# Optimization experiments

Measured on AMD Instinct MI355X. Metric: run time of the kernel, lower is better.

## Reference

```python
import jax, jax.numpy as jnp
import numpy as np
from jax import lax

KS = 2          # kernel_size (even, so padding=ks/2 makes unfold/fold L match)
PAD = 1         # padding = ks//2
STRIDE = 1      # unfold stride
C_IN = 64
PATCH = KS * KS * C_IN  # 256


def unfold(x, ks, stride, pad):
    # torch.nn.functional.unfold ordering: channel-major, then kernel row, kernel col;
    # L axis is row-major over output positions. Output [B, C*ks*ks, L].
    xp = jnp.pad(x, ((0, 0), (0, 0), (pad, pad), (pad, pad)))
    B, C, H, W = xp.shape
    oh = (H - ks) // stride + 1
    ow = (W - ks) // stride + 1
    pats = jnp.stack(
        [xp[:, :, i:i + stride * oh:stride, j:j + stride * ow:stride]
         for i in range(ks) for j in range(ks)], axis=2)  # [B, C, ks*ks, oh, ow]
    return pats.reshape(B, C * ks * ks, oh * ow)


def fold(cols, Ho, Wo, ks, stride, pad):
    # inverse of unfold: scatter-add patch columns back onto an image.
    B, P, L = cols.shape
    C = P // (ks * ks)
    nb = (Ho + 2 * pad - ks) // stride + 1  # blocks per spatial dim
    cols = cols.reshape(B, C, ks, ks, nb, nb)
    out = jnp.zeros((B, C, Ho + 2 * pad, Wo + 2 * pad), dtype=cols.dtype)
    for ki in range(ks):
        for kj in range(ks):
            out = out.at[:, :, ki:ki + stride * nb:stride,
                         kj:kj + stride * nb:stride].add(cols[:, :, ki, kj])
    return out[:, :, pad:pad + Ho, pad:pad + Wo]


def setup_inputs() -> dict:
    key = jax.random.key(0)
    k1, k2, k3, k4 = jax.random.split(key, 4)
    x = jax.random.normal(k1, (32, C_IN, 56, 56), dtype=jnp.float32)
    weight = jax.random.normal(k2, (128, C_IN, KS, KS), dtype=jnp.float32) * 0.06
    bias = jax.random.normal(k3, (128,), dtype=jnp.float32) * 0.06
    cluster_centers = jax.random.uniform(k4, (512, PATCH), dtype=jnp.float32)
    temp = jnp.float32(1.0)
    return {"x": x, "weight": weight, "bias": bias,
            "cluster_centers": cluster_centers, "temp": temp}


def reference(x, weight, bias, cluster_centers, temp):
    B = x.shape[0]
    cols = unfold(x, KS, STRIDE, PAD)                  # [B, 256, L]
    Bc, P, L = cols.shape
    # faithful to torch: this_patch.view(-1, patch_size) on [B, P, L] (row-major)
    flat = cols.reshape(-1, PATCH)                      # [B*L, 256]
    # Euclidean cdist via gram trick
    x2 = jnp.sum(flat * flat, axis=-1, keepdims=True)   # [N,1]
    c2 = jnp.sum(cluster_centers * cluster_centers, axis=-1)  # [K]
    d = jnp.sqrt(jnp.maximum(x2 + c2 - 2.0 * (flat @ cluster_centers.T), 0.0))
    soft = jax.nn.softmax(-d * temp, axis=1)             # [N, K]
    transformed = soft @ cluster_centers                 # [N, 256]
    final = (temp * transformed + flat) / (temp + 1.0)
    final = final.reshape(Bc, P, L)
    new_size = x.shape[3] * KS                           # 112
    x_refold = fold(final, new_size, new_size, KS, KS, PAD)
    # F.conv2d(x_refold, weight, bias, stride=ks, padding=pad, dilation=groups=1)
    out = lax.conv_general_dilated(
        x_refold, weight, window_strides=(KS, KS),
        padding=[(PAD, PAD), (PAD, PAD)],
        dimension_numbers=("NCHW", "OIHW", "NCHW"))
    return out + bias[None, :, None, None]
```

## Files before the change

kernel.cpp:

```cpp
#include <hip/hip_runtime.h>
#include <stdint.h>

#define NB    32
#define CIN   64
#define HW    56
#define OHW   57
#define LL    3249
#define PATCH 256
#define NCENT 512
#define OC    128
#define NROWS (NB*LL)
#define NROWS_PAD 104064
#define PL    (PATCH*LL)

typedef __attribute__((ext_vector_type(8))) short short8;
typedef __attribute__((ext_vector_type(4))) float f32x4;
typedef __attribute__((ext_vector_type(4))) int   int4v;
typedef int int4u __attribute__((ext_vector_type(4), aligned(4)));
typedef __attribute__((ext_vector_type(4))) unsigned short ushort4v;
typedef __attribute__((ext_vector_type(8))) unsigned short ushort8;

constexpr size_t OFF_C2   = 0;
constexpr size_t OFF_X2   = 4096;
constexpr size_t OFF_DENP = OFF_X2 + (size_t)NROWS_PAD*4;
constexpr size_t OFF_DEN  = OFF_DENP + (size_t)8*NROWS_PAD*4;
constexpr size_t OFF_CBF  = OFF_DEN + (size_t)NROWS_PAD*4;
constexpr size_t OFF_CTBF = OFF_CBF + (size_t)NCENT*PATCH*2;
constexpr size_t OFF_WBF  = OFF_CTBF + (size_t)PATCH*NCENT*2;
constexpr size_t OFF_FLAT = OFF_WBF + (size_t)OC*PATCH*2;
constexpr size_t OFF_P    = OFF_FLAT + (size_t)NROWS_PAD*PATCH*2;
constexpr size_t OFF_FBM  = OFF_P + (size_t)NROWS_PAD*NCENT*2;

__device__ __forceinline__ short f2bf(float f) {
    union { float f; uint32_t u; } v; v.f = f;
    uint32_t r = (v.u + 0x7FFFu + ((v.u >> 16) & 1u)) >> 16;
    return (short)r;
}
__device__ __forceinline__ float bf2f(uint16_t h) {
    union { uint32_t u; float f; } v; v.u = ((uint32_t)h) << 16;
    return v.f;
}
__device__ __forceinline__ void gload16(const void* g, void* l) {
    __builtin_amdgcn_global_load_lds(
        (const __attribute__((address_space(1))) unsigned int*)g,
        (__attribute__((address_space(3))) unsigned int*)l, 16, 0, 0);
}

__global__ __launch_bounds__(256)
void k0a_centers(const float* __restrict__ centers, uint16_t* __restrict__ cbf,
                 uint16_t* __restrict__ ctbf, float* __restrict__ c2) {
    __shared__ float red[4];
    int c = blockIdx.x;
    int k = threadIdx.x;
    float v = centers[c*PATCH + k];
    cbf[c*PATCH + (k ^ ((c & 3) << 3))] = (uint16_t)f2bf(v);
    ctbf[k*NCENT + (c ^ ((k & 3) << 3))] = (uint16_t)f2bf(v);
    float s = v*v;
    s += __shfl_xor(s, 1);  s += __shfl_xor(s, 2);  s += __shfl_xor(s, 4);
    s += __shfl_xor(s, 8);  s += __shfl_xor(s, 16); s += __shfl_xor(s, 32);
    int w = threadIdx.x >> 6;
    if ((threadIdx.x & 63) == 0) red[w] = s;
    __syncthreads();
    if (threadIdx.x == 0) c2[c] = red[0] + red[1] + red[2] + red[3];
}

__global__ __launch_bounds__(256)
void k0w_weight(const float* __restrict__ weight, uint16_t* __restrict__ wbf) {
    int o = blockIdx.x, p = threadIdx.x;
    wbf[o*PATCH + (p ^ ((o & 7) << 3))] = (uint16_t)f2bf(weight[o*PATCH + p]);
}

__global__ __launch_bounds__(256)
void k0b_flat(const float* __restrict__ x, uint16_t* __restrict__ flat,
              float* __restrict__ x2) {
    int tid = threadIdx.x;
    int w = tid >> 6, lane = tid & 63;
    for (int pp = 0; pp < 8; ++pp) {
        int n = blockIdx.x*32 + pp*4 + w;
        int b = n / LL;
        int rr = n - b*LL;
        int k0 = lane*4;
        float s = 0.f;
        ushort4v pk;
#pragma unroll
        for (int e = 0; e < 4; ++e) {
            int k = k0 + e;
            float val = 0.f;
            if (n < NROWS) {
                int o = rr*PATCH + k;
                int p = o / LL; int l = o - p*LL;
                int cc = p >> 2, ki = (p >> 1) & 1, kj = p & 1;
                int i = l / OHW; int j = l - i*OHW;
                int y = i + ki - 1, xx = j + kj - 1;
                if ((unsigned)y < HW && (unsigned)xx < HW)
                    val = x[((b*CIN + cc)*HW + y)*HW + xx];
            }
            pk[e] = (unsigned short)f2bf(val);
            s += val*val;
        }
        *(ushort4v*)(flat + (size_t)n*PATCH + (k0 ^ ((n & 3) << 3))) = pk;
        s += __shfl_xor(s, 1);  s += __shfl_xor(s, 2);  s += __shfl_xor(s, 4);
        s += __shfl_xor(s, 8);  s += __shfl_xor(s, 16); s += __shfl_xor(s, 32);
        if (lane == 0) x2[n] = s;
    }
}

__global__ __launch_bounds__(256, 4)
void k1_scores(const uint16_t* __restrict__ flat, const uint16_t* __restrict__ cbf,
               const float* __restrict__ x2g, const float* __restrict__ c2g,
               const float* __restrict__ temp_p,
               uint16_t* __restrict__ P, float* __restrict__ denp) {
    __shared__ __align__(16) char lds[32768];
    const int tid = threadIdx.x;
    const int mt = blockIdx.x, nt = blockIdx.y;
    const int w = tid >> 6, lane = tid & 63;
    const int wr = w >> 1, wc = w & 1;
    const int l15 = lane & 15, l4 = lane >> 4;

    auto stage = [&](int buf, int kt) {
        const char* srcA = (const char*)flat + (size_t)(mt*128)*512 + kt*64;
        const char* srcB = (const char*)cbf + (size_t)(nt*128)*512 + kt*64;
        char* dA = lds + buf*16384;
        char* dB = dA + 8192;
#pragma unroll
        for (int i = 0; i < 2; ++i) {
            int u = (w*2 + i)*64 + lane;
            int row = u >> 2, sub = u & 3;
            gload16(srcA + (size_t)row*512 + sub*16, dA + u*16);
            gload16(srcB + (size_t)row*512 + sub*16, dB + u*16);
        }
    };

    f32x4 acc[4][4];
#pragma unroll
    for (int i = 0; i < 4; ++i)
#pragma unroll
        for (int j = 0; j < 4; ++j) acc[i][j] = (f32x4)0.f;

    stage(0, 0);
    for (int kt = 0; kt < 8; ++kt) {
        __syncthreads();
        if (kt < 7) stage((kt + 1) & 1, kt + 1);
        const char* A = lds + (kt & 1)*16384;
        const char* B = A + 8192;
        short8 af[4], bfm[4];
#pragma unroll
        for (int rf = 0; rf < 4; ++rf) {
            int row = wr*64 + rf*16 + l15;
            int byte = row*64 + ((l4*16) ^ ((row & 3) << 4));
            af[rf] = *(const short8*)(A + byte);
        }
#pragma unroll
        for (int cf = 0; cf < 4; ++cf) {
            int row = wc*64 + cf*16 + l15;
            int byte = row*64 + ((l4*16) ^ ((row & 3) << 4));
            bfm[cf] = *(const short8*)(B + byte);
        }
#pragma unroll
        for (int rf = 0; rf < 4; ++rf)
#pragma unroll
            for (int cf = 0; cf < 4; ++cf)
                acc[rf][cf] = __builtin_amdgcn_mfma_f32_16x16x32_bf16(
                    af[rf], bfm[cf], acc[rf][cf], 0, 0, 0);
    }

    const float temp = temp_p[0];
    float c2v[4];
#pragma unroll
    for (int cf = 0; cf < 4; ++cf)
        c2v[cf] = c2g[nt*128 + wc*64 + cf*16 + l15];

    float denacc[4][4];
#pragma unroll
    for (int rf = 0; rf < 4; ++rf) {
#pragma unroll
        for (int rr = 0; rr < 4; ++rr) {
            int n = mt*128 + wr*64 + rf*16 + l4*4 + rr;
            float x2v = x2g[n];
            float d = 0.f;
#pragma unroll
            for (int cf = 0; cf < 4; ++cf) {
                float s = x2v + c2v[cf] - 2.f*acc[rf][cf][rr];
                float pv = __expf(-temp * sqrtf(fmaxf(s, 0.f)));
                acc[rf][cf][rr] = pv;
                d += pv;
            }
            denacc[rf][rr] = d;
        }
    }
#pragma unroll
    for (int rf = 0; rf < 4; ++rf)
#pragma unroll
        for (int rr = 0; rr < 4; ++rr) {
            float v = denacc[rf][rr];
            v += __shfl_xor(v, 1); v += __shfl_xor(v, 2);
            v += __shfl_xor(v, 4); v += __shfl_xor(v, 8);
            if (l15 == 0) {
                int n = mt*128 + wr*64 + rf*16 + l4*4 + rr;
                denp[(size_t)(nt*2 + wc)*NROWS_PAD + n] = v;
            }
        }

    __syncthreads();
    uint16_t* Pl = (uint16_t*)lds;
#pragma unroll
    for (int rf = 0; rf < 4; ++rf)
#pragma unroll
        for (int cf = 0; cf < 4; ++cf)
#pragma unroll
            for (int rr = 0; rr < 4; ++rr) {
                int row = wr*64 + rf*16 + l4*4 + rr;
                int cl  = wc*64 + cf*16 + l15;
                Pl[row*128 + (cl ^ ((row & 3) << 3))] = (uint16_t)f2bf(acc[rf][cf][rr]);
            }
    __syncthreads();
#pragma unroll
    for (int i = 0; i < 8; ++i) {
        int c = i*256 + tid;
        int row = c >> 4, sub = c & 15;
        int4v v = *(const int4v*)((const char*)lds + c*16);
        *(int4v*)((char*)P + (size_t)(mt*128 + row)*1024 + nt*256 + sub*16) = v;
    }
}

__global__ __launch_bounds__(128)
void kden(const float* __restrict__ denp, float* __restrict__ den) {
    int n = blockIdx.x*128 + threadIdx.x;
    float s = 0.f;
#pragma unroll
    for (int p = 0; p < 8; ++p) s += denp[(size_t)p*NROWS_PAD + n];
    den[n] = s;
}

__global__ __launch_bounds__(256, 4)
void k2_pv(const uint16_t* __restrict__ P, const uint16_t* __restrict__ ctbf,
           const uint16_t* __restrict__ flat, const float* __restrict__ den,
           const float* __restrict__ temp_p, uint16_t* __restrict__ fbm) {
    __shared__ __align__(16) char lds[32768];
    const int tid = threadIdx.x;
    const int mt = blockIdx.x, nt = blockIdx.y;
    const int w = tid >> 6, lane = tid & 63;
    const int wr = w >> 1, wc = w & 1;
    const int l15 = lane & 15, l4 = lane >> 4;

    auto stage = [&](int buf, int kt) {
        const char* srcA = (const char*)P + (size_t)(mt*128)*1024 + kt*64;
        const char* srcB = (const char*)ctbf + (size_t)(nt*128)*1024 + kt*64;
        char* dA = lds + buf*16384;
        char* dB = dA + 8192;
#pragma unroll
        for (int i = 0; i < 2; ++i) {
            int u = (w*2 + i)*64 + lane;
            int row = u >> 2, sub = u & 3;
            gload16(srcA + (size_t)row*1024 + sub*16, dA + u*16);
            gload16(srcB + (size_t)row*1024 + sub*16, dB + u*16);
        }
    };

    f32x4 acc[4][4];
#pragma unroll
    for (int i = 0; i < 4; ++i)
#pragma unroll
        for (int j = 0; j < 4; ++j) acc[i][j] = (f32x4)0.f;

    stage(0, 0);
    for (int kt = 0; kt < 16; ++kt) {
        __syncthreads();
        if (kt < 15) stage((kt + 1) & 1, kt + 1);
        const char* A = lds + (kt & 1)*16384;
        const char* B = A + 8192;
        short8 af[4], bfm[4];
#pragma unroll
        for (int rf = 0; rf < 4; ++rf) {
            int row = wr*64 + rf*16 + l15;
            int byte = row*64 + ((l4*16) ^ ((row & 3) << 4));
            af[rf] = *(const short8*)(A + byte);
        }
#pragma unroll
        for (int cf = 0; cf < 4; ++cf) {
            int row = wc*64 + cf*16 + l15;
            int byte = row*64 + ((l4*16) ^ ((row & 3) << 4));
            bfm[cf] = *(const short8*)(B + byte);
        }
#pragma unroll
        for (int rf = 0; rf < 4; ++rf)
#pragma unroll
            for (int cf = 0; cf < 4; ++cf)
                acc[rf][cf] = __builtin_amdgcn_mfma_f32_16x16x32_bf16(
                    af[rf], bfm[cf], acc[rf][cf], 0, 0, 0);
    }

    __syncthreads();
    uint16_t* Tl = (uint16_t*)lds;
#pragma unroll
    for (int rf = 0; rf < 4; ++rf)
#pragma unroll
        for (int cf = 0; cf < 4; ++cf)
#pragma unroll
            for (int rr = 0; rr < 4; ++rr) {
                int row = wr*64 + rf*16 + l4*4 + rr;
                int col = wc*64 + cf*16 + l15;
                Tl[row*128 + (col ^ ((row & 7) << 3))] = (uint16_t)f2bf(acc[rf][cf][rr]);
            }
    __syncthreads();

    const float temp = temp_p[0];
    const float inv = 1.f / (temp + 1.f);
#pragma unroll
    for (int i = 0; i < 8; ++i) {
        int ch = i*256 + tid;
        int row = ch >> 4, m0 = (ch & 15)*8;
        int n = mt*128 + row;
        if (n >= NROWS) continue;
        int m = nt*128 + m0;
        float dv = den[n];
        float a1 = temp * inv / dv;
        ushort8 tvv = *(const ushort8*)(Tl + row*128 + (m0 ^ ((row & 7) << 3)));
        ushort8 fl = *(const ushort8*)(flat + (size_t)n*PATCH + (m ^ ((row & 3) << 3)));
        int b = n / LL;
        int rrow = n - b*LL;
        int o = rrow*PATCH + m;
        int p = o / LL; int l = o - p*LL;
        int ii = l / OHW; int jj = l - ii*OHW;
        ushort8 outv;
#pragma unroll
        for (int e = 0; e < 8; ++e) {
            int ki = (p >> 1) & 1, kj = p & 1;
            bool bad = (ii == 0 && ki == 0) || (ii == 56 && ki == 1) ||
                       (jj == 0 && kj == 0) || (jj == 56 && kj == 1);
            float fin = a1*bf2f(tvv[e]) + bf2f(fl[e])*inv;
            outv[e] = bad ? (unsigned short)0 : (unsigned short)f2bf(fin);
            if (++jj == OHW) { jj = 0; if (++ii == OHW) { ii = 0; ++p; } }
        }
        *(ushort8*)(fbm + (size_t)n*PATCH + m) = outv;
    }
}

__global__ __launch_bounds__(256, 2)
void k4_conv(const uint16_t* __restrict__ wbf, const uint16_t* __restrict__ fbm,
             const float* __restrict__ bias, float* __restrict__ out) {
    __shared__ __align__(16) char lds[2][32768];
    const int tid = threadIdx.x;
    const int lt = blockIdx.x;
    const int bb = blockIdx.y;
    const int w = tid >> 6, lane = tid & 63;
    const int wr = w >> 1, wc = w & 1;
    const int l15 = lane & 15, l4 = lane >> 4;

    auto stageA = [&](int buf, int kt) {
        const char* srcA = (const char*)wbf + kt*128;
        char* dA = lds[buf];
#pragma unroll
        for (int i = 0; i < 4; ++i) {
            int c = (w*4 + i)*64 + lane;
            gload16(srcA + (size_t)(c >> 3)*512 + (c & 7)*16, dA + (w*4 + i)*1024);
        }
    };
    auto stageB = [&](int buf, int kt) {
        uint16_t* sB = (uint16_t*)(lds[buf] + 16384);
#pragma unroll
        for (int i = 0; i < 4; ++i) {
            int pl = lane;
            int l8 = i*4 + w;
            const uint16_t* g = fbm + (size_t)bb*PL + (size_t)(kt*64 + pl)*LL + lt*128 + l8*8;
#pragma unroll
            for (int e = 0; e < 8; ++e) {
                uint16_t val = g[e];
                int llocal = l8*8 + e;
                sB[llocal*64 + (pl ^ (e << 3))] = val;
            }
        }
    };

    f32x4 acc[4][4];
#pragma unroll
    for (int i = 0; i < 4; ++i)
#pragma unroll
        for (int j = 0; j < 4; ++j) acc[i][j] = (f32x4)0.f;

    stageA(0, 0); stageB(0, 0);
    for (int kt = 0; kt < 4; ++kt) {
        __syncthreads();
        if (kt < 3) { stageA((kt + 1) & 1, kt + 1); stageB((kt + 1) & 1, kt + 1); }
        const char* A = lds[kt & 1];
        const char* B = lds[kt & 1] + 16384;
#pragma unroll
        for (int ks = 0; ks < 2; ++ks) {
            short8 af[4], bfm[4];
#pragma unroll
            for (int rf = 0; rf < 4; ++rf) {
                int row = wr*64 + rf*16 + l15;
                int byte = row*128 + ((ks*64 + l4*16) ^ ((row & 7) << 4));
                af[rf] = *(const short8*)(A + byte);
            }
#pragma unroll
            for (int cf = 0; cf < 4; ++cf) {
                int row = wc*64 + cf*16 + l15;
                int byte = row*128 + ((ks*64 + l4*16) ^ ((row & 7) << 4));
                bfm[cf] = *(const short8*)(B + byte);
            }
#pragma unroll
            for (int rf = 0; rf < 4; ++rf)
#pragma unroll
                for (int cf = 0; cf < 4; ++cf)
                    acc[rf][cf] = __builtin_amdgcn_mfma_f32_16x16x32_bf16(
                        af[rf], bfm[cf], acc[rf][cf], 0, 0, 0);
        }
    }

    __syncthreads();
    float* Ol = (float*)lds;
    float bv[4][4];
#pragma unroll
    for (int rf = 0; rf < 4; ++rf)
#pragma unroll
        for (int rr = 0; rr < 4; ++rr)
            bv[rf][rr] = bias[wr*64 + rf*16 + l4*4 + rr];
#pragma unroll
    for (int rf = 0; rf < 4; ++rf)
#pragma unroll
        for (int cf = 0; cf < 4; ++cf)
#pragma unroll
            for (int rr = 0; rr < 4; ++rr) {
                int row = wr*64 + rf*16 + l4*4 + rr;
                int col = wc*64 + cf*16 + l15;
                Ol[row*128 + col] = acc[rf][cf][rr] + bv[rf][rr];
            }
    __syncthreads();
    if (lt < 25) {
#pragma unroll
        for (int i = 0; i < 16; ++i) {
            int c = i*256 + tid;
            int row = c >> 5, sub = c & 31;
            int4u v = *(const int4u*)((const char*)lds + c*16);
            *(int4u*)((char*)out + ((size_t)(bb*OC + row)*LL + lt*128 + sub*4)*4) = v;
        }
    } else {
#pragma unroll
        for (int i = 0; i < 16; ++i) {
            int c = i*256 + tid;
            int row = c >> 5, sub = c & 31;
            const float* vp = (const float*)((const char*)lds + c*16);
#pragma unroll
            for (int e = 0; e < 4; ++e) {
                int l = lt*128 + sub*4 + e;
                if (l < LL) out[(size_t)(bb*OC + row)*LL + l] = vp[e];
            }
        }
    }
}

extern "C" void kernel_launch(void* const* d_in, const int* in_sizes, int n_in,
                              void* d_out, int out_size, void* d_ws, size_t ws_size,
                              hipStream_t stream) {
    const float* x       = (const float*)d_in[0];
    const float* weight  = (const float*)d_in[1];
    const float* bias    = (const float*)d_in[2];
    const float* centers = (const float*)d_in[3];
    const float* temp    = (const float*)d_in[4];
    float* out = (float*)d_out;

    char* ws = (char*)d_ws;
    float*    c2   = (float*)(ws + OFF_C2);
    float*    x2   = (float*)(ws + OFF_X2);
    float*    denp = (float*)(ws + OFF_DENP);
    float*    den  = (float*)(ws + OFF_DEN);
    uint16_t* cbf  = (uint16_t*)(ws + OFF_CBF);
    uint16_t* ctbf = (uint16_t*)(ws + OFF_CTBF);
    uint16_t* wbf  = (uint16_t*)(ws + OFF_WBF);
    uint16_t* flat = (uint16_t*)(ws + OFF_FLAT);
    uint16_t* P    = (uint16_t*)(ws + OFF_P);
    uint16_t* fbm  = (uint16_t*)(ws + OFF_FBM);

    k0a_centers<<<NCENT, 256, 0, stream>>>(centers, cbf, ctbf, c2);
    k0w_weight<<<OC, 256, 0, stream>>>(weight, wbf);
    k0b_flat<<<NROWS_PAD/32, 256, 0, stream>>>(x, flat, x2);
    k1_scores<<<dim3(NROWS_PAD/128, 4), 256, 0, stream>>>(flat, cbf, x2, c2, temp, P, denp);
    kden<<<NROWS_PAD/128, 128, 0, stream>>>(denp, den);
    k2_pv<<<dim3(NROWS_PAD/128, 2), 256, 0, stream>>>(P, ctbf, flat, den, temp, fbm);
    k4_conv<<<dim3(26, NB), 256, 0, stream>>>(wbf, fbm, bias, out);
}
```

Before: 224.7 us.

## Halve conv kernel LDS footprint to raise occupancy and use HIP bf16 conversion

The final conv GEMM kernel now stages K in 32-wide chunks over 8 iterations instead of 64-wide over 4. This halves LDS to 32KB, and launch bounds are raised to allow 4 blocks per CU. The epilogue writes output through LDS in two 64-row halves so the smaller buffer fits. The weight swizzle changes to match the new 64-byte row stride, and the manual float-to-bf16 rounding is replaced with the HIP intrinsic. The trade-off is more barriers per tile and more register pressure under the tighter launch bound.

```diff
diff --git a/kernel.cpp b/kernel.cpp
--- a/kernel.cpp
+++ b/kernel.cpp
@@ -1,4 +1,5 @@
 #include <hip/hip_runtime.h>
+#include <hip/hip_bf16.h>
 #include <stdint.h>
 
 #define NB    32
@@ -31,10 +32,10 @@
 constexpr size_t OFF_P    = OFF_FLAT + (size_t)NROWS_PAD*PATCH*2;
 constexpr size_t OFF_FBM  = OFF_P + (size_t)NROWS_PAD*NCENT*2;
 
-__device__ __forceinline__ short f2bf(float f) {
-    union { float f; uint32_t u; } v; v.f = f;
-    uint32_t r = (v.u + 0x7FFFu + ((v.u >> 16) & 1u)) >> 16;
-    return (short)r;
+__device__ __forceinline__ unsigned short f2bf(float f) {
+    __hip_bfloat16 h = __float2bfloat16(f);
+    union { __hip_bfloat16 h; unsigned short u; } v; v.h = h;
+    return v.u;
 }
 __device__ __forceinline__ float bf2f(uint16_t h) {
     union { uint32_t u; float f; } v; v.u = ((uint32_t)h) << 16;
@@ -53,8 +54,8 @@
     int c = blockIdx.x;
     int k = threadIdx.x;
     float v = centers[c*PATCH + k];
-    cbf[c*PATCH + (k ^ ((c & 3) << 3))] = (uint16_t)f2bf(v);
-    ctbf[k*NCENT + (c ^ ((k & 3) << 3))] = (uint16_t)f2bf(v);
+    cbf[c*PATCH + (k ^ ((c & 3) << 3))] = f2bf(v);
+    ctbf[k*NCENT + (c ^ ((k & 3) << 3))] = f2bf(v);
     float s = v*v;
     s += __shfl_xor(s, 1);  s += __shfl_xor(s, 2);  s += __shfl_xor(s, 4);
     s += __shfl_xor(s, 8);  s += __shfl_xor(s, 16); s += __shfl_xor(s, 32);
@@ -67,7 +68,7 @@
 __global__ __launch_bounds__(256)
 void k0w_weight(const float* __restrict__ weight, uint16_t* __restrict__ wbf) {
     int o = blockIdx.x, p = threadIdx.x;
-    wbf[o*PATCH + (p ^ ((o & 7) << 3))] = (uint16_t)f2bf(weight[o*PATCH + p]);
+    wbf[o*PATCH + (p ^ ((o & 3) << 3))] = f2bf(weight[o*PATCH + p]);
 }
 
 __global__ __launch_bounds__(256)
@@ -95,7 +96,7 @@
                 if ((unsigned)y < HW && (unsigned)xx < HW)
                     val = x[((b*CIN + cc)*HW + y)*HW + xx];
             }
-            pk[e] = (unsigned short)f2bf(val);
+            pk[e] = f2bf(val);
             s += val*val;
         }
         *(ushort4v*)(flat + (size_t)n*PATCH + (k0 ^ ((n & 3) << 3))) = pk;
@@ -329,17 +330,17 @@
             bool bad = (ii == 0 && ki == 0) || (ii == 56 && ki == 1) ||
                        (jj == 0 && kj == 0) || (jj == 56 && kj == 1);
             float fin = a1*bf2f(tvv[e]) + bf2f(fl[e])*inv;
-            outv[e] = bad ? (unsigned short)0 : (unsigned short)f2bf(fin);
+            outv[e] = bad ? (unsigned short)0 : f2bf(fin);
             if (++jj == OHW) { jj = 0; if (++ii == OHW) { ii = 0; ++p; } }
         }
         *(ushort8*)(fbm + (size_t)n*PATCH + m) = outv;
     }
 }
 
-__global__ __launch_bounds__(256, 2)
+__global__ __launch_bounds__(256, 4)
 void k4_conv(const uint16_t* __restrict__ wbf, const uint16_t* __restrict__ fbm,
              const float* __restrict__ bias, float* __restrict__ out) {
-    __shared__ __align__(16) char lds[2][32768];
+    __shared__ __align__(16) char lds[32768];
     const int tid = threadIdx.x;
     const int lt = blockIdx.x;
     const int bb = blockIdx.y;
@@ -348,26 +349,27 @@
     const int l15 = lane & 15, l4 = lane >> 4;
 
     auto stageA = [&](int buf, int kt) {
-        const char* srcA = (const char*)wbf + kt*128;
-        char* dA = lds[buf];
-#pragma unroll
-        for (int i = 0; i < 4; ++i) {
-            int c = (w*4 + i)*64 + lane;
-            gload16(srcA + (size_t)(c >> 3)*512 + (c & 7)*16, dA + (w*4 + i)*1024);
+        const char* srcA = (const char*)wbf + kt*64;
+        char* dA = lds + buf*16384;
+#pragma unroll
+        for (int i = 0; i < 2; ++i) {
+            int u = i*256 + tid;
+            int row = u >> 2, sub = u & 3;
+            gload16(srcA + (size_t)row*512 + sub*16, dA + u*16);
         }
     };
     auto stageB = [&](int buf, int kt) {
-        uint16_t* sB = (uint16_t*)(lds[buf] + 16384);
-#pragma unroll
-        for (int i = 0; i < 4; ++i) {
-            int pl = lane;
-            int l8 = i*4 + w;
-            const uint16_t* g = fbm + (size_t)bb*PL + (size_t)(kt*64 + pl)*LL + lt*128 + l8*8;
+        uint16_t* sB = (uint16_t*)(lds + buf*16384 + 8192);
+        int pl = lane & 31;
+        int lh = lane >> 5;
+#pragma unroll
+        for (int i = 0; i < 2; ++i) {
+            int l8 = i*8 + w*2 + lh;
+            const uint16_t* g = fbm + (size_t)bb*PL + (size_t)(kt*32 + pl)*LL + lt*128 + l8*8;
 #pragma unroll
             for (int e = 0; e < 8; ++e) {
-                uint16_t val = g[e];
                 int llocal = l8*8 + e;
-                sB[llocal*64 + (pl ^ (e << 3))] = val;
+                sB[llocal*32 + (pl ^ ((llocal & 3) << 3))] = g[e];
             }
         }
     };
@@ -379,72 +381,75 @@
         for (int j = 0; j < 4; ++j) acc[i][j] = (f32x4)0.f;
 
     stageA(0, 0); stageB(0, 0);
-    for (int kt = 0; kt < 4; ++kt) {
+    for (int kt = 0; kt < 8; ++kt) {
         __syncthreads();
-        if (kt < 3) { stageA((kt + 1) & 1, kt + 1); stageB((kt + 1) & 1, kt + 1); }
-        const char* A = lds[kt & 1];
-        const char* B = lds[kt & 1] + 16384;
-#pragma unroll
-        for (int ks = 0; ks < 2; ++ks) {
-            short8 af[4], bfm[4];
-#pragma unroll
-            for (int rf = 0; rf < 4; ++rf) {
-                int row = wr*64 + rf*16 + l15;
-                int byte = row*128 + ((ks*64 + l4*16) ^ ((row & 7) << 4));
-                af[rf] = *(const short8*)(A + byte);
-            }
-#pragma unroll
-            for (int cf = 0; cf < 4; ++cf) {
-                int row = wc*64 + cf*16 + l15;
-                int byte = row*128 + ((ks*64 + l4*16) ^ ((row & 7) << 4));
-                bfm[cf] = *(const short8*)(B + byte);
-            }
-#pragma unroll
-            for (int rf = 0; rf < 4; ++rf)
-#pragma unroll
-                for (int cf = 0; cf < 4; ++cf)
-                    acc[rf][cf] = __builtin_amdgcn_mfma_f32_16x16x32_bf16(
-                        af[rf], bfm[cf], acc[rf][cf], 0, 0, 0);
-        }
-    }
-
-    __syncthreads();
-    float* Ol = (float*)lds;
+        if (kt < 7) { stageA((kt + 1) & 1, kt + 1); stageB((kt + 1) & 1, kt + 1); }
+        const char* A = lds + (kt & 1)*16384;
+        const char* B = A + 8192;
+        short8 af[4], bfm[4];
+#pragma unroll
+        for (int rf = 0; rf < 4; ++rf) {
+            int row = wr*64 + rf*16 + l15;
+            int byte = row*64 + ((l4*16) ^ ((row & 3) << 4));
+            af[rf] = *(const short8*)(A + byte);
+        }
+#pragma unroll
+        for (int cf = 0; cf < 4; ++cf) {
+            int row = wc*64 + cf*16 + l15;
+            int byte = row*64 + ((l4*16) ^ ((row & 3) << 4));
+            bfm[cf] = *(const short8*)(B + byte);
+        }
+#pragma unroll
+        for (int rf = 0; rf < 4; ++rf)
+#pragma unroll
+            for (int cf = 0; cf < 4; ++cf)
+                acc[rf][cf] = __builtin_amdgcn_mfma_f32_16x16x32_bf16(
+                    af[rf], bfm[cf], acc[rf][cf], 0, 0, 0);
+    }
+
     float bv[4][4];
 #pragma unroll
     for (int rf = 0; rf < 4; ++rf)
 #pragma unroll
         for (int rr = 0; rr < 4; ++rr)
             bv[rf][rr] = bias[wr*64 + rf*16 + l4*4 + rr];
-#pragma unroll
-    for (int rf = 0; rf < 4; ++rf)
-#pragma unroll
-        for (int cf = 0; cf < 4; ++cf)
-#pragma unroll
-            for (int rr = 0; rr < 4; ++rr) {
-                int row = wr*64 + rf*16 + l4*4 + rr;
-                int col = wc*64 + cf*16 + l15;
-                Ol[row*128 + col] = acc[rf][cf][rr] + bv[rf][rr];
-            }
-    __syncthreads();
-    if (lt < 25) {
-#pragma unroll
-        for (int i = 0; i < 16; ++i) {
-            int c = i*256 + tid;
-            int row = c >> 5, sub = c & 31;
-            int4u v = *(const int4u*)((const char*)lds + c*16);
-            *(int4u*)((char*)out + ((size_t)(bb*OC + row)*LL + lt*128 + sub*4)*4) = v;
-        }
-    } else {
-#pragma unroll
-        for (int i = 0; i < 16; ++i) {
-            int c = i*256 + tid;
-            int row = c >> 5, sub = c & 31;
-            const float* vp = (const float*)((const char*)lds + c*16);
-#pragma unroll
-            for (int e = 0; e < 4; ++e) {
-                int l = lt*128 + sub*4 + e;
-                if (l < LL) out[(size_t)(bb*OC + row)*LL + l] = vp[e];
+
+    float* Ol = (float*)lds;
+    for (int half = 0; half < 2; ++half) {
+        __syncthreads();
+        if (wr == half) {
+#pragma unroll
+            for (int rf = 0; rf < 4; ++rf)
+#pragma unroll
+                for (int cf = 0; cf < 4; ++cf)
+#pragma unroll
+                    for (int rr = 0; rr < 4; ++rr) {
+                        int rowl = rf*16 + l4*4 + rr;
+                        int col = wc*64 + cf*16 + l15;
+                        Ol[rowl*128 + col] = acc[rf][cf][rr] + bv[rf][rr];
+                    }
+        }
+        __syncthreads();
+        int base_oc = half*64;
+        if (lt < 25) {
+#pragma unroll
+            for (int i = 0; i < 8; ++i) {
+                int c = i*256 + tid;
+                int row = c >> 5, sub = c & 31;
+                int4u v = *(const int4u*)((const char*)lds + c*16);
+                *(int4u*)((char*)out + ((size_t)(bb*OC + base_oc + row)*LL + lt*128 + sub*4)*4) = v;
+            }
+        } else {
+#pragma unroll
+            for (int i = 0; i < 8; ++i) {
+                int c = i*256 + tid;
+                int row = c >> 5, sub = c & 31;
+                const float* vp = (const float*)((const char*)lds + c*16);
+#pragma unroll
+                for (int e = 0; e < 4; ++e) {
+                    int l = lt*128 + sub*4 + e;
+                    if (l < LL) out[(size_t)(bb*OC + base_oc + row)*LL + l] = vp[e];
+                }
             }
         }
     }
```

After: 219.9 us. -2.2%, faster.
